# Performance work log

Measured on AMD Instinct MI355X. Metric: run time of the kernel, lower is better.

The kernel has to match this reference:

```python
import jax, jax.numpy as jnp
import numpy as np
from jax import lax

N, IC, OC, K, SDIM, H, W = 16, 512, 512, 3, 512, 32, 32
PAD, STRIDE, LR = 1, 1, 1.0
WEIGHT_SCALER = 1.0 / np.sqrt(IC * K * K) * LR   # equalized-lr conv scale
FC_SCALER = 1.0 / np.sqrt(SDIM) * LR             # equalized-lr fc scale


def setup_inputs() -> dict:
    key = jax.random.key(0)
    k1, k2, k3 = jax.random.split(key, 3)
    x = jax.random.normal(k1, (N, IC, H, W), dtype=jnp.float32)
    style = jax.random.normal(k2, (N, SDIM), dtype=jnp.float32)
    weight = jax.random.normal(k3, (OC, IC, K, K), dtype=jnp.float32)  # std = 1/lr = 1
    fc_weight = jax.random.normal(jax.random.fold_in(key, 10), (IC, SDIM), dtype=jnp.float32)
    fc_bias = jnp.zeros((IC,), dtype=jnp.float32)
    return {"x": x, "style": style, "weight": weight,
            "fc_weight": fc_weight, "fc_bias": fc_bias}


def reference(x, style, weight, fc_weight, fc_bias):
    # EqualizedFullyConnect + AddChannelwiseBias, then +1 -> modulation rates [N, iC]
    mod = jnp.einsum('ns,cs->nc', style, fc_weight) * FC_SCALER + fc_bias * LR + 1.0
    # modulated per-sample weight [N, oC, iC, kH, kW]
    w = WEIGHT_SCALER * weight[None] * mod[:, None, :, None, None]
    # demodulate: rsqrt of sum of squares over (iC, kH, kW)
    demod = lax.rsqrt(jnp.sum(w * w, axis=(2, 3, 4)) + 1e-8)  # [N, oC]
    w = w * demod[:, :, None, None, None]
    # grouped conv with groups=N == per-sample conv: vmap over batch
    def conv1(xi, wi):
        # xi: [iC,H,W], wi: [oC,iC,kH,kW]
        return lax.conv_general_dilated(
            xi[None], wi, window_strides=(STRIDE, STRIDE),
            padding=((PAD, PAD), (PAD, PAD)),
            dimension_numbers=('NCHW', 'OIHW', 'NCHW'))[0]
    out = jax.vmap(conv1)(x, w)  # [N, oC, H, W]
    return out
```

## Files before the change

kernel.cpp:

```cpp
#include <hip/hip_runtime.h>
#include <hip/hip_bf16.h>

#define N_    16
#define IC_   512
#define OC_   512
#define SDIM_ 512
#define H_    32
#define W_    32
#define HW_   1024

#define FC_SCALER 0.04419417382415922f
#define WS_       0.014731391274719738f
#define WS2_      (1.0f/4608.0f)

typedef __attribute__((__ext_vector_type__(8)))  __bf16 bf16x8;
typedef __attribute__((__ext_vector_type__(16))) float  f32x16;
typedef __attribute__((__ext_vector_type__(4)))  int    i32x4;

typedef __attribute__((address_space(1))) const unsigned int GInt;
typedef __attribute__((address_space(3))) unsigned int LInt;

#define WAIT3()  asm volatile("s_waitcnt vmcnt(3)"  ::: "memory")
#define WAIT43() asm volatile("s_waitcnt vmcnt(43)" ::: "memory")
#define WAIT46() asm volatile("s_waitcnt vmcnt(46)" ::: "memory")
#define WAIT0()  asm volatile("s_waitcnt vmcnt(0)"  ::: "memory")
#define LGKM0()  asm volatile("s_waitcnt lgkmcnt(0)" ::: "memory")
#define SB()     __builtin_amdgcn_sched_barrier(0)

__device__ __forceinline__ unsigned short f2bf(float f) {
    unsigned int u = __builtin_bit_cast(unsigned int, f);
    unsigned int r = (u + 0x7FFFu + ((u >> 16) & 1u)) >> 16;
    return (unsigned short)r;
}

__global__ void k_mod(const float* __restrict__ style, const float* __restrict__ fcw,
                      const float* __restrict__ fcb, float* __restrict__ mod) {
    int gid = blockIdx.x * blockDim.x + threadIdx.x;
    int wid = gid >> 6, lane = gid & 63;
    if (wid >= N_ * IC_) return;
    int n = wid >> 9, c = wid & 511;
    const float4* sp = (const float4*)(style + n * SDIM_);
    const float4* wp = (const float4*)(fcw + (size_t)c * SDIM_);
    float acc = 0.f;
    for (int i = lane; i < SDIM_ / 4; i += 64) {
        float4 a = sp[i], b = wp[i];
        acc += a.x*b.x + a.y*b.y + a.z*b.z + a.w*b.w;
    }
#pragma unroll
    for (int off = 32; off; off >>= 1) acc += __shfl_xor(acc, off);
    if (lane == 0) mod[wid] = acc * FC_SCALER + fcb[c] + 1.0f;
}

__global__ void k_wprep(const float* __restrict__ w, unsigned short* __restrict__ wt,
                        float* __restrict__ wsq) {
    int tid = blockIdx.x * blockDim.x + threadIdx.x;
    int oc = tid >> 9, ic = tid & 511;
    int og = oc >> 6, ocl = oc & 63;
    int icc = ic >> 5, ks = (ic >> 3) & 3, i8 = ic & 7;
    float s = 0.f;
#pragma unroll
    for (int t = 0; t < 9; t++) {
        float v = w[(size_t)tid * 9 + t];
        s += v * v;
        size_t off = (((size_t)t * 8 + og) * 16 + icc) * 2048
                   + (size_t)ks * 512 + ocl * 8 + i8;
        wt[off] = f2bf(v);
    }
    wsq[tid] = s;
}

__global__ void k_demod(const float* __restrict__ mod, const float* __restrict__ wsq,
                        float* __restrict__ demod_ws) {
    int gid = blockIdx.x * blockDim.x + threadIdx.x;
    int wid = gid >> 6, lane = gid & 63;
    if (wid >= N_ * OC_) return;
    int n = wid >> 9, oc = wid & 511;
    const float4* mp = (const float4*)(mod + n * IC_);
    const float4* qp = (const float4*)(wsq + (size_t)oc * IC_);
    float acc = 0.f;
    for (int i = lane; i < IC_ / 4; i += 64) {
        float4 m = mp[i], q = qp[i];
        acc += m.x*m.x*q.x + m.y*m.y*q.y + m.z*m.z*q.z + m.w*m.w*q.w;
    }
#pragma unroll
    for (int off = 32; off; off >>= 1) acc += __shfl_xor(acc, off);
    if (lane == 0) {
        float s = WS2_ * acc + 1e-8f;
        demod_ws[wid] = WS_ / sqrtf(s);
    }
}

__global__ __launch_bounds__(256, 2)
void k_conv(const float* __restrict__ x, const float* __restrict__ mod,
            const unsigned short* __restrict__ wt,
            const float* __restrict__ demod_ws, float* __restrict__ out) {
    __shared__ __align__(16) char smem[81184];
    unsigned short* xt0     = (unsigned short*)(smem);
    unsigned short* wb0     = (unsigned short*)(smem + 40960);
    unsigned short* trash   = (unsigned short*)(smem + 77824);
    float*          zslot   = (float*)(smem + 78848);
    float*          s_demod = (float*)(smem + 78880);
    float*          mod_lds = (float*)(smem + 79136);

    int bx = blockIdx.x;
    int x8 = bx & 7, jj = bx >> 3;
    int n = x8 * 2 + (jj >> 5);
    int rem = jj & 31;
    int octg = rem >> 2, spt = rem & 3;
    int oc0 = octg * 64, y0 = spt * 8;

    int tid = threadIdx.x, lane = tid & 63, wid = tid >> 6;
    int l31 = lane & 31, lhi = lane >> 5;
    int wc = wid & 1, kh = wid >> 1;

    if (tid < 64) s_demod[tid] = demod_ws[n * OC_ + oc0 + tid];
    if (tid < 128) ((float4*)mod_lds)[tid] = ((const float4*)(mod + n * IC_))[tid];
    if (tid == 0) { i32x4 z = {}; *(i32x4*)zslot = z; }
    SB();

    const float* xsrc = x + (size_t)n * IC_ * HW_;

    float xr[5][8];
    auto stage_xregs = [&](int icc) {
#pragma unroll
        for (int k = 0; k < 5; k++) {
            int rr = lhi + 2 * k;
            int y = y0 - 1 + rr;
            int yc = y < 0 ? 0 : (y > 31 ? 31 : y);
            const float* base = xsrc + ((size_t)(icc * 32 + wid * 8)) * HW_ + yc * 32 + l31;
#pragma unroll
            for (int i = 0; i < 8; i++) xr[k][i] = base[(size_t)i * HW_];
        }
    };
    auto cvt_store = [&](int icct, int buf) {
        int mi = (icct & 15) * 32 + wid * 8;
        float4 mA = *(const float4*)&mod_lds[mi];
        float4 mB = *(const float4*)&mod_lds[mi + 4];
#pragma unroll
        for (int k = 0; k < 5; k++) {
            int rr = lhi + 2 * k;
            int y = y0 - 1 + rr;
            bool oob = (unsigned)y >= 32u;
            unsigned r0 = 0, r1 = 0, r2 = 0, r3 = 0;
            if (!oob) {
                float f0 = xr[k][0]*mA.x, f1 = xr[k][1]*mA.y;
                float f2 = xr[k][2]*mA.z, f3 = xr[k][3]*mA.w;
                float f4 = xr[k][4]*mB.x, f5 = xr[k][5]*mB.y;
                float f6 = xr[k][6]*mB.z, f7 = xr[k][7]*mB.w;
                asm("v_cvt_pk_bf16_f32 %0, %1, %2" : "=v"(r0) : "v"(f0), "v"(f1));
                asm("v_cvt_pk_bf16_f32 %0, %1, %2" : "=v"(r1) : "v"(f2), "v"(f3));
                asm("v_cvt_pk_bf16_f32 %0, %1, %2" : "=v"(r2) : "v"(f4), "v"(f5));
                asm("v_cvt_pk_bf16_f32 %0, %1, %2" : "=v"(r3) : "v"(f6), "v"(f7));
            }
            i32x4 v = { (int)r0, (int)r1, (int)r2, (int)r3 };
            *(i32x4*)(xt0 + buf * 10240 + rr * 1024 + wid * 256 + l31 * 8) = v;
        }
    };
    auto stage_w = [&](int g2) {
        int gc = g2 < 48 ? g2 : 47;
        int icc2 = gc / 3, p2 = gc % 3;
        bool oob = g2 >= 48;
#pragma unroll
        for (int k = 0; k < 3; k++) {
            int tap = k * 3 + p2;
            const unsigned short* g =
                wt + (((size_t)tap * 8 + octg) * 16 + icc2) * 2048 + wid * 512 + lane * 8;
            unsigned short* l = oob ? trash
                                    : wb0 + (g2 % 3) * 6144 + k * 2048 + wid * 512;
            __builtin_amdgcn_global_load_lds((GInt*)g, (LInt*)l, 16, 0, 0);
        }
    };

    f32x16 acc[2][4] = {};
    int xb = 0;
    int kso = kh * 2 + lhi;

    auto compute = [&](int p, const unsigned short* wbp) {
        const unsigned short* xtb = xt0 + xb * 10240;
        int col = l31 + p - 1;
        bool oobc = (unsigned)col >= 32u;
        bf16x8 r6[6];
#pragma unroll
        for (int j = 0; j < 6; j++) {
            int rr = wc * 4 + j;
            const unsigned short* src = oobc ? (const unsigned short*)zslot
                : xtb + rr * 1024 + kso * 256 + col * 8;
            r6[j] = *(const bf16x8*)src;
        }
#pragma unroll
        for (int dy = 0; dy < 3; dy++) {
            bf16x8 af0 = *(const bf16x8*)(wbp + dy * 2048 + kso * 512 + l31 * 8);
            bf16x8 af1 = *(const bf16x8*)(wbp + dy * 2048 + kso * 512 + (32 + l31) * 8);
            __builtin_amdgcn_s_setprio(1);
#pragma unroll
            for (int fs = 0; fs < 4; fs++)
                acc[0][fs] = __builtin_amdgcn_mfma_f32_32x32x16_bf16(
                    af0, r6[fs + dy], acc[0][fs], 0, 0, 0);
#pragma unroll
            for (int fs = 0; fs < 4; fs++)
                acc[1][fs] = __builtin_amdgcn_mfma_f32_32x32x16_bf16(
                    af1, r6[fs + dy], acc[1][fs], 0, 0, 0);
            __builtin_amdgcn_s_setprio(0);
        }
    };

    stage_xregs(0); SB();
    float x0r[5][8];
#pragma unroll
    for (int k = 0; k < 5; k++)
#pragma unroll
        for (int i = 0; i < 8; i++) x0r[k][i] = xr[k][i];
    stage_xregs(1); SB();
    stage_w(0); stage_w(1); SB();
    WAIT46();
    LGKM0();
    __builtin_amdgcn_s_barrier();
    {
        int mi = 0 * 32 + wid * 8;
        float4 mA = *(const float4*)&mod_lds[mi];
        float4 mB = *(const float4*)&mod_lds[mi + 4];
#pragma unroll
        for (int k = 0; k < 5; k++) {
            int rr = lhi + 2 * k;
            int y = y0 - 1 + rr;
            bool oob = (unsigned)y >= 32u;
            unsigned r0 = 0, r1 = 0, r2 = 0, r3 = 0;
            if (!oob) {
                float f0 = x0r[k][0]*mA.x, f1 = x0r[k][1]*mA.y;
                float f2 = x0r[k][2]*mA.z, f3 = x0r[k][3]*mA.w;
                float f4 = x0r[k][4]*mB.x, f5 = x0r[k][5]*mB.y;
                float f6 = x0r[k][6]*mB.z, f7 = x0r[k][7]*mB.w;
                asm("v_cvt_pk_bf16_f32 %0, %1, %2" : "=v"(r0) : "v"(f0), "v"(f1));
                asm("v_cvt_pk_bf16_f32 %0, %1, %2" : "=v"(r1) : "v"(f2), "v"(f3));
                asm("v_cvt_pk_bf16_f32 %0, %1, %2" : "=v"(r2) : "v"(f4), "v"(f5));
                asm("v_cvt_pk_bf16_f32 %0, %1, %2" : "=v"(r3) : "v"(f6), "v"(f7));
            }
            i32x4 v = { (int)r0, (int)r1, (int)r2, (int)r3 };
            *(i32x4*)(xt0 + rr * 1024 + wid * 256 + l31 * 8) = v;
        }
    }
    SB();

#pragma unroll 1
    for (int icc = 0; icc < 16; icc++) {
        int g0 = icc * 3;
        WAIT3();
        LGKM0();
        __builtin_amdgcn_s_barrier();
        cvt_store(icc + 1, xb ^ 1);
        SB();
        stage_w(g0 + 2);
        SB();
        stage_xregs((icc + 2) & 15);
        SB();
        compute(0, wb0 + (g0 % 3) * 6144);
        WAIT43();
        LGKM0();
        __builtin_amdgcn_s_barrier();
        stage_w(g0 + 3);
        SB();
        compute(1, wb0 + ((g0 + 1) % 3) * 6144);
        WAIT43();
        LGKM0();
        __builtin_amdgcn_s_barrier();
        stage_w(g0 + 4);
        SB();
        compute(2, wb0 + ((g0 + 2) % 3) * 6144);
        xb ^= 1;
    }

    WAIT0();
    __syncthreads();
    float* exch = (float*)smem;
    if (kh == 1) {
#pragma unroll
        for (int fo = 0; fo < 2; fo++)
#pragma unroll
            for (int fs = 0; fs < 4; fs++)
#pragma unroll
                for (int rg = 0; rg < 16; rg++)
                    exch[(((wc * 2 + fo) * 4 + fs) * 16 + rg) * 64 + lane] = acc[fo][fs][rg];
    }
    __syncthreads();
    if (kh == 0) {
#pragma unroll
        for (int fo = 0; fo < 2; fo++) {
#pragma unroll
            for (int fs = 0; fs < 4; fs++) {
                int y = y0 + wc * 4 + fs;
#pragma unroll
                for (int rg = 0; rg < 16; rg++) {
                    int row = (rg & 3) + 8 * (rg >> 2) + 4 * lhi;
                    int ocl = fo * 32 + row;
                    float v = acc[fo][fs][rg]
                            + exch[(((wc * 2 + fo) * 4 + fs) * 16 + rg) * 64 + lane];
                    v *= s_demod[ocl];
                    out[((size_t)(n * OC_ + oc0 + ocl) * H_ + y) * W_ + l31] = v;
                }
            }
        }
    }
}

extern "C" void kernel_launch(void* const* d_in, const int* in_sizes, int n_in,
                              void* d_out, int out_size, void* d_ws, size_t ws_size,
                              hipStream_t stream) {
    const float* x      = (const float*)d_in[0];
    const float* style  = (const float*)d_in[1];
    const float* weight = (const float*)d_in[2];
    const float* fcw    = (const float*)d_in[3];
    const float* fcb    = (const float*)d_in[4];
    float* out = (float*)d_out;

    char* ws = (char*)d_ws;
    float*          mod   = (float*)ws;
    float*          demod = (float*)(ws + 32768);
    float*          wsq   = (float*)(ws + 65536);
    unsigned short* wtb   = (unsigned short*)(ws + 65536 + 1048576);

    k_mod   <<<2048, 256, 0, stream>>>(style, fcw, fcb, mod);
    k_wprep <<<1024, 256, 0, stream>>>(weight, wtb, wsq);
    k_demod <<<2048, 256, 0, stream>>>(mod, wsq, demod);
    k_conv  <<<512,  256, 0, stream>>>(x, mod, wtb, demod, out);
}
```

Measured before the change: 99.71 us.

## Load conv weights directly into registers instead of staging through LDS

Replaces the triple-buffered global_load_lds weight staging with per-lane direct global loads into registers, double-buffered across conv column taps. This cuts LDS usage roughly in half, from about 81KB to 43KB, and removes two of the three barriers per input-channel chunk. The final cross-wave reduction is split into two passes to fit the smaller LDS. The cost is more VGPR pressure and reliance on compiler-inserted vmcnt waits, so weight load latency may be exposed before the MFMAs.

```diff
diff --git a/kernel.cpp b/kernel.cpp
--- a/kernel.cpp
+++ b/kernel.cpp
@@ -17,13 +17,6 @@
 typedef __attribute__((__ext_vector_type__(16))) float  f32x16;
 typedef __attribute__((__ext_vector_type__(4)))  int    i32x4;
 
-typedef __attribute__((address_space(1))) const unsigned int GInt;
-typedef __attribute__((address_space(3))) unsigned int LInt;
-
-#define WAIT3()  asm volatile("s_waitcnt vmcnt(3)"  ::: "memory")
-#define WAIT43() asm volatile("s_waitcnt vmcnt(43)" ::: "memory")
-#define WAIT46() asm volatile("s_waitcnt vmcnt(46)" ::: "memory")
-#define WAIT0()  asm volatile("s_waitcnt vmcnt(0)"  ::: "memory")
 #define LGKM0()  asm volatile("s_waitcnt lgkmcnt(0)" ::: "memory")
 #define SB()     __builtin_amdgcn_sched_barrier(0)
 
@@ -94,13 +87,11 @@
 void k_conv(const float* __restrict__ x, const float* __restrict__ mod,
             const unsigned short* __restrict__ wt,
             const float* __restrict__ demod_ws, float* __restrict__ out) {
-    __shared__ __align__(16) char smem[81184];
+    __shared__ __align__(16) char smem[43360];
     unsigned short* xt0     = (unsigned short*)(smem);
-    unsigned short* wb0     = (unsigned short*)(smem + 40960);
-    unsigned short* trash   = (unsigned short*)(smem + 77824);
-    float*          zslot   = (float*)(smem + 78848);
-    float*          s_demod = (float*)(smem + 78880);
-    float*          mod_lds = (float*)(smem + 79136);
+    float*          zslot   = (float*)(smem + 40960);
+    float*          s_demod = (float*)(smem + 40992);
+    float*          mod_lds = (float*)(smem + 41248);
 
     int bx = blockIdx.x;
     int x8 = bx & 7, jj = bx >> 3;
@@ -112,11 +103,11 @@
     int tid = threadIdx.x, lane = tid & 63, wid = tid >> 6;
     int l31 = lane & 31, lhi = lane >> 5;
     int wc = wid & 1, kh = wid >> 1;
+    int kso = kh * 2 + lhi;
 
     if (tid < 64) s_demod[tid] = demod_ws[n * OC_ + oc0 + tid];
     if (tid < 128) ((float4*)mod_lds)[tid] = ((const float4*)(mod + n * IC_))[tid];
     if (tid == 0) { i32x4 z = {}; *(i32x4*)zslot = z; }
-    SB();
 
     const float* xsrc = x + (size_t)n * IC_ * HW_;
 
@@ -156,26 +147,23 @@
             *(i32x4*)(xt0 + buf * 10240 + rr * 1024 + wid * 256 + l31 * 8) = v;
         }
     };
-    auto stage_w = [&](int g2) {
+    auto fetch_w = [&](int g2, bf16x8 (&dst)[6]) {
         int gc = g2 < 48 ? g2 : 47;
-        int icc2 = gc / 3, p2 = gc % 3;
-        bool oob = g2 >= 48;
-#pragma unroll
-        for (int k = 0; k < 3; k++) {
-            int tap = k * 3 + p2;
-            const unsigned short* g =
-                wt + (((size_t)tap * 8 + octg) * 16 + icc2) * 2048 + wid * 512 + lane * 8;
-            unsigned short* l = oob ? trash
-                                    : wb0 + (g2 % 3) * 6144 + k * 2048 + wid * 512;
-            __builtin_amdgcn_global_load_lds((GInt*)g, (LInt*)l, 16, 0, 0);
+        int icc2 = gc / 3, p2 = gc - icc2 * 3;
+#pragma unroll
+        for (int dy = 0; dy < 3; dy++) {
+            int tap = dy * 3 + p2;
+            const unsigned short* base =
+                wt + (((size_t)tap * 8 + octg) * 16 + icc2) * 2048 + kso * 512 + l31 * 8;
+            dst[dy * 2 + 0] = *(const bf16x8*)(base);
+            dst[dy * 2 + 1] = *(const bf16x8*)(base + 256);
         }
     };
 
     f32x16 acc[2][4] = {};
     int xb = 0;
-    int kso = kh * 2 + lhi;
-
-    auto compute = [&](int p, const unsigned short* wbp) {
+
+    auto compute = [&](int p, const bf16x8 (&wAv)[6]) {
         const unsigned short* xtb = xt0 + xb * 10240;
         int col = l31 + p - 1;
         bool oobc = (unsigned)col >= 32u;
@@ -189,102 +177,65 @@
         }
 #pragma unroll
         for (int dy = 0; dy < 3; dy++) {
-            bf16x8 af0 = *(const bf16x8*)(wbp + dy * 2048 + kso * 512 + l31 * 8);
-            bf16x8 af1 = *(const bf16x8*)(wbp + dy * 2048 + kso * 512 + (32 + l31) * 8);
             __builtin_amdgcn_s_setprio(1);
 #pragma unroll
             for (int fs = 0; fs < 4; fs++)
                 acc[0][fs] = __builtin_amdgcn_mfma_f32_32x32x16_bf16(
-                    af0, r6[fs + dy], acc[0][fs], 0, 0, 0);
+                    wAv[dy * 2 + 0], r6[fs + dy], acc[0][fs], 0, 0, 0);
 #pragma unroll
             for (int fs = 0; fs < 4; fs++)
                 acc[1][fs] = __builtin_amdgcn_mfma_f32_32x32x16_bf16(
-                    af1, r6[fs + dy], acc[1][fs], 0, 0, 0);
+                    wAv[dy * 2 + 1], r6[fs + dy], acc[1][fs], 0, 0, 0);
             __builtin_amdgcn_s_setprio(0);
         }
     };
 
-    stage_xregs(0); SB();
-    float x0r[5][8];
-#pragma unroll
-    for (int k = 0; k < 5; k++)
-#pragma unroll
-        for (int i = 0; i < 8; i++) x0r[k][i] = xr[k][i];
-    stage_xregs(1); SB();
-    stage_w(0); stage_w(1); SB();
-    WAIT46();
+    bf16x8 wA0[6], wA1[6];
+
+    stage_xregs(0);
+    fetch_w(0, wA0);
+    __syncthreads();
+    cvt_store(0, 0);
+    stage_xregs(1);
     LGKM0();
     __builtin_amdgcn_s_barrier();
-    {
-        int mi = 0 * 32 + wid * 8;
-        float4 mA = *(const float4*)&mod_lds[mi];
-        float4 mB = *(const float4*)&mod_lds[mi + 4];
-#pragma unroll
-        for (int k = 0; k < 5; k++) {
-            int rr = lhi + 2 * k;
-            int y = y0 - 1 + rr;
-            bool oob = (unsigned)y >= 32u;
-            unsigned r0 = 0, r1 = 0, r2 = 0, r3 = 0;
-            if (!oob) {
-                float f0 = x0r[k][0]*mA.x, f1 = x0r[k][1]*mA.y;
-                float f2 = x0r[k][2]*mA.z, f3 = x0r[k][3]*mA.w;
-                float f4 = x0r[k][4]*mB.x, f5 = x0r[k][5]*mB.y;
-                float f6 = x0r[k][6]*mB.z, f7 = x0r[k][7]*mB.w;
-                asm("v_cvt_pk_bf16_f32 %0, %1, %2" : "=v"(r0) : "v"(f0), "v"(f1));
-                asm("v_cvt_pk_bf16_f32 %0, %1, %2" : "=v"(r1) : "v"(f2), "v"(f3));
-                asm("v_cvt_pk_bf16_f32 %0, %1, %2" : "=v"(r2) : "v"(f4), "v"(f5));
-                asm("v_cvt_pk_bf16_f32 %0, %1, %2" : "=v"(r3) : "v"(f6), "v"(f7));
-            }
-            i32x4 v = { (int)r0, (int)r1, (int)r2, (int)r3 };
-            *(i32x4*)(xt0 + rr * 1024 + wid * 256 + l31 * 8) = v;
-        }
-    }
     SB();
 
-#pragma unroll 1
-    for (int icc = 0; icc < 16; icc++) {
+    auto icc_body = [&](int icc, bf16x8 (&sA)[6], bf16x8 (&sB)[6]) {
         int g0 = icc * 3;
-        WAIT3();
+        fetch_w(g0 + 1, sB);
+        compute(0, sA);
+        fetch_w(g0 + 2, sA);
+        if (icc < 15) cvt_store(icc + 1, xb ^ 1);
+        stage_xregs(icc + 2 <= 15 ? icc + 2 : 0);
+        compute(1, sB);
+        fetch_w(g0 + 3, sB);
+        compute(2, sA);
         LGKM0();
         __builtin_amdgcn_s_barrier();
-        cvt_store(icc + 1, xb ^ 1);
         SB();
-        stage_w(g0 + 2);
-        SB();
-        stage_xregs((icc + 2) & 15);
-        SB();
-        compute(0, wb0 + (g0 % 3) * 6144);
-        WAIT43();
-        LGKM0();
-        __builtin_amdgcn_s_barrier();
-        stage_w(g0 + 3);
-        SB();
-        compute(1, wb0 + ((g0 + 1) % 3) * 6144);
-        WAIT43();
-        LGKM0();
-        __builtin_amdgcn_s_barrier();
-        stage_w(g0 + 4);
-        SB();
-        compute(2, wb0 + ((g0 + 2) % 3) * 6144);
         xb ^= 1;
-    }
-
-    WAIT0();
+    };
+
+#pragma unroll 1
+    for (int ii = 0; ii < 8; ii++) {
+        icc_body(2 * ii,     wA0, wA1);
+        icc_body(2 * ii + 1, wA1, wA0);
+    }
+
     __syncthreads();
     float* exch = (float*)smem;
-    if (kh == 1) {
-#pragma unroll
-        for (int fo = 0; fo < 2; fo++)
+#pragma unroll
+    for (int fo = 0; fo < 2; fo++) {
+        if (kh == 1) {
 #pragma unroll
             for (int fs = 0; fs < 4; fs++)
 #pragma unroll
                 for (int rg = 0; rg < 16; rg++)
-                    exch[(((wc * 2 + fo) * 4 + fs) * 16 + rg) * 64 + lane] = acc[fo][fs][rg];
-    }
-    __syncthreads();
-    if (kh == 0) {
-#pragma unroll
-        for (int fo = 0; fo < 2; fo++) {
+                    exch[((wc * 4 + fs) * 16 + rg) * 64 + lane] = acc[fo][fs][rg];
+        }
+        __syncthreads();
+        if (kh == 0) {
 #pragma unroll
             for (int fs = 0; fs < 4; fs++) {
                 int y = y0 + wc * 4 + fs;
@@ -293,12 +244,13 @@
                     int row = (rg & 3) + 8 * (rg >> 2) + 4 * lhi;
                     int ocl = fo * 32 + row;
                     float v = acc[fo][fs][rg]
-                            + exch[(((wc * 2 + fo) * 4 + fs) * 16 + rg) * 64 + lane];
+                            + exch[((wc * 4 + fs) * 16 + rg) * 64 + lane];
                     v *= s_demod[ocl];
                     out[((size_t)(n * OC_ + oc0 + ocl) * H_ + y) * W_ + l31] = v;
                 }
             }
         }
+        __syncthreads();
     }
 }
 
```

Result: slower. 159.5 us (+60.0%).
